# Kernel optimization log

Measured on AMD Instinct MI355X. Metric: run time of the kernel, lower is better.

Reference implementation:

```python
import jax, jax.numpy as jnp
import numpy as np

B, C, T = 32, 64, 8192
OUT, K = 129, 32
TWO_PI = 2.0 * np.pi
DROP_THRESH = 0.1  # squared-distance threshold for channel dropping


def setup_inputs() -> dict:
    key = jax.random.key(0)
    k1, k2, k3, k4, k5 = jax.random.split(key, 5)
    X = jax.random.normal(k1, (B, C, T), dtype=jnp.float32)
    positions = jax.random.uniform(k2, (B, C, 2), dtype=jnp.float32)
    drop_idx = jax.random.randint(k3, (B,), 0, C)
    scale = 1.0 / (K * K)
    z_real = jax.random.normal(k4, (OUT, K * K), dtype=jnp.float32) * scale
    z_imag = jax.random.normal(k5, (OUT, K * K), dtype=jnp.float32) * scale
    return {"X": X, "positions": positions, "drop_idx": drop_idx,
            "z_real": z_real, "z_imag": z_imag}


def reference(X, positions, drop_idx, z_real, z_imag):
    # frequency grid: feature index f = l_idx*K + k_idx (row-major over [l, k])
    kk = jnp.arange(1, K + 1, dtype=jnp.float32)
    coef_k = jnp.tile(kk, K)            # [K*K] varies fastest
    coef_l = jnp.repeat(kk, K)          # [K*K]

    x = positions[..., 0]               # [B, C]
    y = positions[..., 1]
    # phase: [B, C, K*K]
    phase = TWO_PI * (x[..., None] * coef_k + y[..., None] * coef_l)
    cos_mat = jnp.cos(phase)
    sin_mat = jnp.sin(phase)

    # a: [B, OUT, C]
    a = (jnp.einsum('of,bcf->boc', z_real, cos_mat)
         + jnp.einsum('of,bcf->boc', z_imag, sin_mat))

    # channel drop: remove all channels within sqdist < 0.1 of the dropped electrode
    pd = positions[jnp.arange(B), drop_idx]                 # [B, 2]
    dist = jnp.sum((positions - pd[:, None, :]) ** 2, axis=-1)  # [B, C]
    keep = dist >= DROP_THRESH                              # [B, C]

    a = jnp.where(keep[:, None, :], a, -1e9)
    attn = jax.nn.softmax(a, axis=2)                        # [B, OUT, C]
    # out: [B, OUT, T]
    return jnp.einsum('boc,bct->bot', attn, X)
```

## Files before the change

kernel.cpp:

```cpp
#include <hip/hip_runtime.h>
#include <math.h>

typedef __bf16 bf16x8 __attribute__((ext_vector_type(8)));
typedef unsigned short u16x8 __attribute__((ext_vector_type(8)));
typedef float f32x4 __attribute__((ext_vector_type(4)));

namespace {
constexpr int kB   = 32;
constexpr int kC   = 64;
constexpr int kT   = 8192;
constexpr int kOUT = 129;
constexpr int kKK  = 1024;
constexpr int kNKC = 8;
}

__device__ inline float sin2pi(float r) {
  float o; asm("v_sin_f32 %0, %1" : "=v"(o) : "v"(r)); return o;
}
__device__ inline float cos2pi(float r) {
  float o; asm("v_cos_f32 %0, %1" : "=v"(o) : "v"(r)); return o;
}
__device__ inline unsigned short f2bf_rne(float f) {
  unsigned int u = __builtin_bit_cast(unsigned int, f);
  return (unsigned short)((u + 0x7fffu + ((u >> 16) & 1u)) >> 16);
}
__device__ inline float bf2f(unsigned short h) {
  return __builtin_bit_cast(float, (unsigned int)h << 16);
}
__device__ inline void split8(const float* v, bf16x8& hi, bf16x8& lo) {
  u16x8 h, l;
#pragma unroll
  for (int j = 0; j < 8; ++j) {
    const unsigned short hh = f2bf_rne(v[j]);
    h[j] = hh;
    l[j] = f2bf_rne(v[j] - bf2f(hh));
  }
  hi = __builtin_bit_cast(bf16x8, h);
  lo = __builtin_bit_cast(bf16x8, l);
}

__global__ __launch_bounds__(256) void sa_phase_mfma(
    const float* __restrict__ positions,
    const float* __restrict__ z_real,
    const float* __restrict__ z_imag,
    float* __restrict__ part)
{
  const int bid = blockIdx.x;
  const int b   = bid & 31;
  const int kc  = (bid >> 5) & 7;
  const int mh  = bid >> 8;
  const int w    = threadIdx.x >> 6;
  const int lane = threadIdx.x & 63;
  const int cg   = lane >> 4;
  const int cl   = lane & 15;
  const int c    = w * 16 + cl;
  const int f0   = kc * 128;

  const float2 p = reinterpret_cast<const float2*>(positions)[b * kC + c];

  bf16x8 BcH[4], BcL[4], BsH[4], BsL[4];
#pragma unroll
  for (int ks = 0; ks < 4; ++ks) {
    float cs[8], sn[8];
#pragma unroll
    for (int j = 0; j < 8; ++j) {
      const int f = f0 + ks * 32 + 8 * cg + j;
      const float kf = (float)((f & 31) + 1);
      const float lf = (float)((f >> 5) + 1);
      const float wv = __fadd_rn(__fmul_rn(p.x, kf), __fmul_rn(p.y, lf));
      const float r  = wv - floorf(wv);
      cs[j] = cos2pi(r);
      sn[j] = sin2pi(r);
    }
    split8(cs, BcH[ks], BcL[ks]);
    split8(sn, BsH[ks], BsL[ks]);
  }

  const int nm  = mh ? 4 : 5;
  const int ob0 = mh * 80;

#pragma unroll
  for (int m = 0; m < 5; ++m) {
    if (m < nm) {
      const int ob = ob0 + m * 16;
      const int oa = ob + cl;
      bf16x8 ArH[4], ArL[4], AiH[4], AiL[4];
      if (oa < kOUT) {
        const float* zr = z_real + (size_t)oa * kKK + f0 + 8 * cg;
        const float* zi = z_imag + (size_t)oa * kKK + f0 + 8 * cg;
#pragma unroll
        for (int ks = 0; ks < 4; ++ks) {
          float vr[8], vi[8];
          *reinterpret_cast<float4*>(vr)     = *reinterpret_cast<const float4*>(zr + ks * 32);
          *reinterpret_cast<float4*>(vr + 4) = *reinterpret_cast<const float4*>(zr + ks * 32 + 4);
          *reinterpret_cast<float4*>(vi)     = *reinterpret_cast<const float4*>(zi + ks * 32);
          *reinterpret_cast<float4*>(vi + 4) = *reinterpret_cast<const float4*>(zi + ks * 32 + 4);
          split8(vr, ArH[ks], ArL[ks]);
          split8(vi, AiH[ks], AiL[ks]);
        }
      } else {
#pragma unroll
        for (int ks = 0; ks < 4; ++ks) {
          u16x8 z0 = {0,0,0,0,0,0,0,0};
          ArH[ks] = ArL[ks] = AiH[ks] = AiL[ks] = __builtin_bit_cast(bf16x8, z0);
        }
      }

      f32x4 acc = {0.f, 0.f, 0.f, 0.f};
#pragma unroll
      for (int ks = 0; ks < 4; ++ks) {
        acc = __builtin_amdgcn_mfma_f32_16x16x32_bf16(ArH[ks], BcH[ks], acc, 0, 0, 0);
        acc = __builtin_amdgcn_mfma_f32_16x16x32_bf16(ArH[ks], BcL[ks], acc, 0, 0, 0);
        acc = __builtin_amdgcn_mfma_f32_16x16x32_bf16(ArL[ks], BcH[ks], acc, 0, 0, 0);
        acc = __builtin_amdgcn_mfma_f32_16x16x32_bf16(AiH[ks], BsH[ks], acc, 0, 0, 0);
        acc = __builtin_amdgcn_mfma_f32_16x16x32_bf16(AiH[ks], BsL[ks], acc, 0, 0, 0);
        acc = __builtin_amdgcn_mfma_f32_16x16x32_bf16(AiL[ks], BsH[ks], acc, 0, 0, 0);
      }

#pragma unroll
      for (int r = 0; r < 4; ++r) {
        const int o = ob + cg * 4 + r;
        if (o < kOUT)
          part[(((size_t)kc * kB + b) * kOUT + o) * kC + c] = acc[r];
      }
    }
  }
}

__global__ __launch_bounds__(64) void sa_softmax(
    const float* __restrict__ part,
    const float* __restrict__ positions,
    const int*   __restrict__ drop_idx,
    unsigned short* __restrict__ a_hi,
    unsigned short* __restrict__ a_lo)
{
  const int bo = blockIdx.x;
  const int b  = bo / kOUT;
  const int o  = bo - b * kOUT;
  const int c  = threadIdx.x;

  float a = 0.f;
#pragma unroll
  for (int fc = 0; fc < kNKC; ++fc)
    a += part[(((size_t)fc * kB + b) * kOUT + o) * kC + c];

  const float2 p  = reinterpret_cast<const float2*>(positions)[b * kC + c];
  const int    di = drop_idx[b];
  const float2 pd = reinterpret_cast<const float2*>(positions)[b * kC + di];
  const float dx = p.x - pd.x;
  const float dy = p.y - pd.y;
  const float d2 = __fadd_rn(__fmul_rn(dx, dx), __fmul_rn(dy, dy));
  if (d2 < 0.1f) a = -1e9f;

  float m = a;
#pragma unroll
  for (int off = 32; off; off >>= 1) m = fmaxf(m, __shfl_xor(m, off));
  const float e = expf(a - m);
  float s = e;
#pragma unroll
  for (int off = 32; off; off >>= 1) s += __shfl_xor(s, off);

  const float att = e / s;
  const unsigned short h = f2bf_rne(att);
  const float res = att - bf2f(h);
  a_hi[((size_t)b * kOUT + o) * kC + c] = h;
  a_lo[((size_t)b * kOUT + o) * kC + c] = f2bf_rne(res);
}

__global__ __launch_bounds__(256) void sa_apply_mfma(
    const float* __restrict__ X,
    const unsigned short* __restrict__ a_hi,
    const unsigned short* __restrict__ a_lo,
    float* __restrict__ out)
{
  __shared__ unsigned short s_a[2 * 144 * kC];

  const int b   = blockIdx.x >> 6;
  const int tc  = blockIdx.x & 63;
  const int t0  = tc * 128;
  const int tid = threadIdx.x;

  {
    char* sb = reinterpret_cast<char*>(s_a);
    for (int i = tid; i < 2 * 144 * 8; i += 256) {
      const int tile = (i >= 144 * 8) ? 1 : 0;
      const int r    = (i >> 3) - tile * 144;
      const int ch   = i & 7;
      float4 v;
      if (r < kOUT) {
        const unsigned short* src =
            (tile ? a_lo : a_hi) + ((size_t)b * kOUT + r) * kC + ch * 8;
        v = *reinterpret_cast<const float4*>(src);
      } else {
        v = make_float4(0.f, 0.f, 0.f, 0.f);
      }
      const int byte = tile * (144 * 128) + r * 128 + ((ch * 16) ^ ((r & 7) << 4));
      *reinterpret_cast<float4*>(sb + byte) = v;
    }
  }

  const int wave = tid >> 6;
  const int lane = tid & 63;
  const int cl   = lane & 15;
  const int cg   = lane >> 4;
  const int tA   = t0 + wave * 32 + cl;
  const int tB   = tA + 16;

  const float* Xb = X + (size_t)b * kC * kT;
  float xvA[16], xvB[16];
#pragma unroll
  for (int s2 = 0; s2 < 2; ++s2)
#pragma unroll
    for (int j = 0; j < 8; ++j) {
      const size_t row = (size_t)(s2 * 32 + cg * 8 + j) * kT;
      xvA[s2 * 8 + j] = Xb[row + tA];
      xvB[s2 * 8 + j] = Xb[row + tB];
    }

  bf16x8 XhA0, XlA0, XhA1, XlA1, XhB0, XlB0, XhB1, XlB1;
  split8(xvA,     XhA0, XlA0);
  split8(xvA + 8, XhA1, XlA1);
  split8(xvB,     XhB0, XlB0);
  split8(xvB + 8, XhB1, XlB1);

  __syncthreads();

  const char* sb = reinterpret_cast<const char*>(s_a);
  float* outb = out + (size_t)b * kOUT * kT;

  for (int m = 0; m < 9; ++m) {
    const int row  = m * 16 + cl;
    const int base = row * 128;
    const int sw   = (row & 7) << 4;
    const int gb   = cg * 16;

    const bf16x8 Ah0 = *reinterpret_cast<const bf16x8*>(sb + base + ((gb     ) ^ sw));
    const bf16x8 Ah1 = *reinterpret_cast<const bf16x8*>(sb + base + ((gb + 64) ^ sw));
    const bf16x8 Al0 = *reinterpret_cast<const bf16x8*>(sb + 144 * 128 + base + ((gb     ) ^ sw));
    const bf16x8 Al1 = *reinterpret_cast<const bf16x8*>(sb + 144 * 128 + base + ((gb + 64) ^ sw));

    f32x4 accA = {0.f, 0.f, 0.f, 0.f};
    f32x4 accB = {0.f, 0.f, 0.f, 0.f};
    accA = __builtin_amdgcn_mfma_f32_16x16x32_bf16(Ah0, XhA0, accA, 0, 0, 0);
    accB = __builtin_amdgcn_mfma_f32_16x16x32_bf16(Ah0, XhB0, accB, 0, 0, 0);
    accA = __builtin_amdgcn_mfma_f32_16x16x32_bf16(Ah1, XhA1, accA, 0, 0, 0);
    accB = __builtin_amdgcn_mfma_f32_16x16x32_bf16(Ah1, XhB1, accB, 0, 0, 0);
    accA = __builtin_amdgcn_mfma_f32_16x16x32_bf16(Al0, XhA0, accA, 0, 0, 0);
    accB = __builtin_amdgcn_mfma_f32_16x16x32_bf16(Al0, XhB0, accB, 0, 0, 0);
    accA = __builtin_amdgcn_mfma_f32_16x16x32_bf16(Al1, XhA1, accA, 0, 0, 0);
    accB = __builtin_amdgcn_mfma_f32_16x16x32_bf16(Al1, XhB1, accB, 0, 0, 0);
    accA = __builtin_amdgcn_mfma_f32_16x16x32_bf16(Ah0, XlA0, accA, 0, 0, 0);
    accB = __builtin_amdgcn_mfma_f32_16x16x32_bf16(Ah0, XlB0, accB, 0, 0, 0);
    accA = __builtin_amdgcn_mfma_f32_16x16x32_bf16(Ah1, XlA1, accA, 0, 0, 0);
    accB = __builtin_amdgcn_mfma_f32_16x16x32_bf16(Ah1, XlB1, accB, 0, 0, 0);

#pragma unroll
    for (int r = 0; r < 4; ++r) {
      const int o = m * 16 + cg * 4 + r;
      if (o < kOUT) {
        outb[(size_t)o * kT + tA] = accA[r];
        outb[(size_t)o * kT + tB] = accB[r];
      }
    }
  }
}

extern "C" void kernel_launch(void* const* d_in, const int* in_sizes, int n_in,
                              void* d_out, int out_size, void* d_ws, size_t ws_size,
                              hipStream_t stream) {
  (void)in_sizes; (void)n_in; (void)out_size; (void)ws_size;
  const float* X         = (const float*)d_in[0];
  const float* positions = (const float*)d_in[1];
  const int*   drop_idx  = (const int*)d_in[2];
  const float* z_real    = (const float*)d_in[3];
  const float* z_imag    = (const float*)d_in[4];
  float* out = (float*)d_out;

  float* part = (float*)d_ws;
  unsigned short* ahi = (unsigned short*)(part + (size_t)kNKC * kB * kOUT * kC);
  unsigned short* alo = ahi + (size_t)kB * kOUT * kC;

  sa_phase_mfma<<<kB * kNKC * 2, 256, 0, stream>>>(positions, z_real, z_imag, part);
  sa_softmax<<<kB * kOUT, 64, 0, stream>>>(part, positions, drop_idx, ahi, alo);
  sa_apply_mfma<<<kB * 64, 256, 0, stream>>>(X, ahi, alo, out);
}
```

Baseline: 247.0 us.

## Precompute bf16 split operands in separate kernels and widen apply tiles

New measurement: 235.5 us. 1.05x faster.

```diff
diff --git a/kernel.cpp b/kernel.cpp
--- a/kernel.cpp
+++ b/kernel.cpp
@@ -12,6 +12,7 @@
 constexpr int kOUT = 129;
 constexpr int kKK  = 1024;
 constexpr int kNKC = 8;
+constexpr int kOP  = 144;
 }
 
 __device__ inline float sin2pi(float r) {
@@ -38,11 +39,61 @@
   hi = __builtin_bit_cast(bf16x8, h);
   lo = __builtin_bit_cast(bf16x8, l);
 }
-
-__global__ __launch_bounds__(256) void sa_phase_mfma(
+__device__ inline bf16x8 ldbf8(const unsigned short* p) {
+  return __builtin_bit_cast(bf16x8, *reinterpret_cast<const u16x8*>(p));
+}
+
+__global__ __launch_bounds__(256) void sa_split_z(
+    const float* __restrict__ z_real, const float* __restrict__ z_imag,
+    unsigned short* __restrict__ zrh, unsigned short* __restrict__ zrl,
+    unsigned short* __restrict__ zih, unsigned short* __restrict__ zil)
+{
+  const int i = blockIdx.x * 256 + threadIdx.x;
+  if (i >= 128 * kOP * 8) return;
+  const int fj = i & 7;
+  const int o  = (i >> 3) % kOP;
+  const int fb = i / (kOP * 8);
+  const int f  = fb * 8 + fj;
+  float vr = 0.f, vi = 0.f;
+  if (o < kOUT) {
+    vr = z_real[(size_t)o * kKK + f];
+    vi = z_imag[(size_t)o * kKK + f];
+  }
+  unsigned short h = f2bf_rne(vr);
+  zrh[i] = h; zrl[i] = f2bf_rne(vr - bf2f(h));
+  h = f2bf_rne(vi);
+  zih[i] = h; zil[i] = f2bf_rne(vi - bf2f(h));
+}
+
+__global__ __launch_bounds__(256) void sa_cis(
     const float* __restrict__ positions,
-    const float* __restrict__ z_real,
-    const float* __restrict__ z_imag,
+    unsigned short* __restrict__ csh, unsigned short* __restrict__ csl,
+    unsigned short* __restrict__ snh, unsigned short* __restrict__ snl)
+{
+  const int i = blockIdx.x * 256 + threadIdx.x;
+  const int fj = i & 7;
+  const int c  = (i >> 3) & 63;
+  const int fb = (i >> 9) & 127;
+  const int b  = i >> 16;
+  const int f  = fb * 8 + fj;
+  const float2 p = reinterpret_cast<const float2*>(positions)[b * kC + c];
+  const float kf = (float)((f & 31) + 1);
+  const float lf = (float)((f >> 5) + 1);
+  const float w = __fadd_rn(__fmul_rn(p.x, kf), __fmul_rn(p.y, lf));
+  const float r = w - floorf(w);
+  const float cs = cos2pi(r);
+  const float sn = sin2pi(r);
+  unsigned short h = f2bf_rne(cs);
+  csh[i] = h; csl[i] = f2bf_rne(cs - bf2f(h));
+  h = f2bf_rne(sn);
+  snh[i] = h; snl[i] = f2bf_rne(sn - bf2f(h));
+}
+
+__global__ __launch_bounds__(256) void sa_phase_gemm(
+    const unsigned short* __restrict__ zrh, const unsigned short* __restrict__ zrl,
+    const unsigned short* __restrict__ zih, const unsigned short* __restrict__ zil,
+    const unsigned short* __restrict__ csh, const unsigned short* __restrict__ csl,
+    const unsigned short* __restrict__ snh, const unsigned short* __restrict__ snl,
     float* __restrict__ part)
 {
   const int bid = blockIdx.x;
@@ -54,26 +105,15 @@
   const int cg   = lane >> 4;
   const int cl   = lane & 15;
   const int c    = w * 16 + cl;
-  const int f0   = kc * 128;
-
-  const float2 p = reinterpret_cast<const float2*>(positions)[b * kC + c];
 
   bf16x8 BcH[4], BcL[4], BsH[4], BsL[4];
 #pragma unroll
   for (int ks = 0; ks < 4; ++ks) {
-    float cs[8], sn[8];
-#pragma unroll
-    for (int j = 0; j < 8; ++j) {
-      const int f = f0 + ks * 32 + 8 * cg + j;
-      const float kf = (float)((f & 31) + 1);
-      const float lf = (float)((f >> 5) + 1);
-      const float wv = __fadd_rn(__fmul_rn(p.x, kf), __fmul_rn(p.y, lf));
-      const float r  = wv - floorf(wv);
-      cs[j] = cos2pi(r);
-      sn[j] = sin2pi(r);
-    }
-    split8(cs, BcH[ks], BcL[ks]);
-    split8(sn, BsH[ks], BsL[ks]);
+    const size_t off = ((size_t)(b * 128 + kc * 16 + ks * 4 + cg) * kC + c) * 8;
+    BcH[ks] = ldbf8(csh + off);
+    BcL[ks] = ldbf8(csl + off);
+    BsH[ks] = ldbf8(snh + off);
+    BsL[ks] = ldbf8(snl + off);
   }
 
   const int nm  = mh ? 4 : 5;
@@ -84,39 +124,21 @@
     if (m < nm) {
       const int ob = ob0 + m * 16;
       const int oa = ob + cl;
-      bf16x8 ArH[4], ArL[4], AiH[4], AiL[4];
-      if (oa < kOUT) {
-        const float* zr = z_real + (size_t)oa * kKK + f0 + 8 * cg;
-        const float* zi = z_imag + (size_t)oa * kKK + f0 + 8 * cg;
-#pragma unroll
-        for (int ks = 0; ks < 4; ++ks) {
-          float vr[8], vi[8];
-          *reinterpret_cast<float4*>(vr)     = *reinterpret_cast<const float4*>(zr + ks * 32);
-          *reinterpret_cast<float4*>(vr + 4) = *reinterpret_cast<const float4*>(zr + ks * 32 + 4);
-          *reinterpret_cast<float4*>(vi)     = *reinterpret_cast<const float4*>(zi + ks * 32);
-          *reinterpret_cast<float4*>(vi + 4) = *reinterpret_cast<const float4*>(zi + ks * 32 + 4);
-          split8(vr, ArH[ks], ArL[ks]);
-          split8(vi, AiH[ks], AiL[ks]);
-        }
-      } else {
-#pragma unroll
-        for (int ks = 0; ks < 4; ++ks) {
-          u16x8 z0 = {0,0,0,0,0,0,0,0};
-          ArH[ks] = ArL[ks] = AiH[ks] = AiL[ks] = __builtin_bit_cast(bf16x8, z0);
-        }
+      f32x4 acc = {0.f, 0.f, 0.f, 0.f};
+#pragma unroll
+      for (int ks = 0; ks < 4; ++ks) {
+        const size_t zo = ((size_t)(kc * 16 + ks * 4 + cg) * kOP + oa) * 8;
+        const bf16x8 ArH = ldbf8(zrh + zo);
+        const bf16x8 ArL = ldbf8(zrl + zo);
+        const bf16x8 AiH = ldbf8(zih + zo);
+        const bf16x8 AiL = ldbf8(zil + zo);
+        acc = __builtin_amdgcn_mfma_f32_16x16x32_bf16(ArH, BcH[ks], acc, 0, 0, 0);
+        acc = __builtin_amdgcn_mfma_f32_16x16x32_bf16(ArH, BcL[ks], acc, 0, 0, 0);
+        acc = __builtin_amdgcn_mfma_f32_16x16x32_bf16(ArL, BcH[ks], acc, 0, 0, 0);
+        acc = __builtin_amdgcn_mfma_f32_16x16x32_bf16(AiH, BsH[ks], acc, 0, 0, 0);
+        acc = __builtin_amdgcn_mfma_f32_16x16x32_bf16(AiH, BsL[ks], acc, 0, 0, 0);
+        acc = __builtin_amdgcn_mfma_f32_16x16x32_bf16(AiL, BsH[ks], acc, 0, 0, 0);
       }
-
-      f32x4 acc = {0.f, 0.f, 0.f, 0.f};
-#pragma unroll
-      for (int ks = 0; ks < 4; ++ks) {
-        acc = __builtin_amdgcn_mfma_f32_16x16x32_bf16(ArH[ks], BcH[ks], acc, 0, 0, 0);
-        acc = __builtin_amdgcn_mfma_f32_16x16x32_bf16(ArH[ks], BcL[ks], acc, 0, 0, 0);
-        acc = __builtin_amdgcn_mfma_f32_16x16x32_bf16(ArL[ks], BcH[ks], acc, 0, 0, 0);
-        acc = __builtin_amdgcn_mfma_f32_16x16x32_bf16(AiH[ks], BsH[ks], acc, 0, 0, 0);
-        acc = __builtin_amdgcn_mfma_f32_16x16x32_bf16(AiH[ks], BsL[ks], acc, 0, 0, 0);
-        acc = __builtin_amdgcn_mfma_f32_16x16x32_bf16(AiL[ks], BsH[ks], acc, 0, 0, 0);
-      }
-
 #pragma unroll
       for (int r = 0; r < 4; ++r) {
         const int o = ob + cg * 4 + r;
@@ -127,17 +149,18 @@
   }
 }
 
-__global__ __launch_bounds__(64) void sa_softmax(
+__global__ __launch_bounds__(256) void sa_softmax(
     const float* __restrict__ part,
     const float* __restrict__ positions,
     const int*   __restrict__ drop_idx,
     unsigned short* __restrict__ a_hi,
     unsigned short* __restrict__ a_lo)
 {
-  const int bo = blockIdx.x;
-  const int b  = bo / kOUT;
-  const int o  = bo - b * kOUT;
-  const int c  = threadIdx.x;
+  const int bo = blockIdx.x * 4 + (threadIdx.x >> 6);
+  if (bo >= kB * kOUT) return;
+  const int b = bo / kOUT;
+  const int o = bo - b * kOUT;
+  const int c = threadIdx.x & 63;
 
   float a = 0.f;
 #pragma unroll
@@ -162,9 +185,8 @@
 
   const float att = e / s;
   const unsigned short h = f2bf_rne(att);
-  const float res = att - bf2f(h);
-  a_hi[((size_t)b * kOUT + o) * kC + c] = h;
-  a_lo[((size_t)b * kOUT + o) * kC + c] = f2bf_rne(res);
+  a_hi[(size_t)bo * kC + c] = h;
+  a_lo[(size_t)bo * kC + c] = f2bf_rne(att - bf2f(h));
 }
 
 __global__ __launch_bounds__(256) void sa_apply_mfma(
@@ -175,9 +197,9 @@
 {
   __shared__ unsigned short s_a[2 * 144 * kC];
 
-  const int b   = blockIdx.x >> 6;
-  const int tc  = blockIdx.x & 63;
-  const int t0  = tc * 128;
+  const int b   = blockIdx.x >> 5;
+  const int tc  = blockIdx.x & 31;
+  const int t0  = tc * 256;
   const int tid = threadIdx.x;
 
   {
@@ -203,25 +225,22 @@
   const int lane = tid & 63;
   const int cl   = lane & 15;
   const int cg   = lane >> 4;
-  const int tA   = t0 + wave * 32 + cl;
-  const int tB   = tA + 16;
+  const int tb   = t0 + wave * 64;
 
   const float* Xb = X + (size_t)b * kC * kT;
-  float xvA[16], xvB[16];
-#pragma unroll
-  for (int s2 = 0; s2 < 2; ++s2)
-#pragma unroll
-    for (int j = 0; j < 8; ++j) {
-      const size_t row = (size_t)(s2 * 32 + cg * 8 + j) * kT;
-      xvA[s2 * 8 + j] = Xb[row + tA];
-      xvB[s2 * 8 + j] = Xb[row + tB];
-    }
-
-  bf16x8 XhA0, XlA0, XhA1, XlA1, XhB0, XlB0, XhB1, XlB1;
-  split8(xvA,     XhA0, XlA0);
-  split8(xvA + 8, XhA1, XlA1);
-  split8(xvB,     XhB0, XlB0);
-  split8(xvB + 8, XhB1, XlB1);
+  bf16x8 Xh[4][2], Xl[4][2];
+#pragma unroll
+  for (int n = 0; n < 4; ++n) {
+    const int t = tb + n * 16 + cl;
+    float xv[16];
+#pragma unroll
+    for (int s2 = 0; s2 < 2; ++s2)
+#pragma unroll
+      for (int j = 0; j < 8; ++j)
+        xv[s2 * 8 + j] = Xb[(size_t)(s2 * 32 + cg * 8 + j) * kT + t];
+    split8(xv,     Xh[n][0], Xl[n][0]);
+    split8(xv + 8, Xh[n][1], Xl[n][1]);
+  }
 
   __syncthreads();
 
@@ -239,29 +258,26 @@
     const bf16x8 Al0 = *reinterpret_cast<const bf16x8*>(sb + 144 * 128 + base + ((gb     ) ^ sw));
     const bf16x8 Al1 = *reinterpret_cast<const bf16x8*>(sb + 144 * 128 + base + ((gb + 64) ^ sw));
 
-    f32x4 accA = {0.f, 0.f, 0.f, 0.f};
-    f32x4 accB = {0.f, 0.f, 0.f, 0.f};
-    accA = __builtin_amdgcn_mfma_f32_16x16x32_bf16(Ah0, XhA0, accA, 0, 0, 0);
-    accB = __builtin_amdgcn_mfma_f32_16x16x32_bf16(Ah0, XhB0, accB, 0, 0, 0);
-    accA = __builtin_amdgcn_mfma_f32_16x16x32_bf16(Ah1, XhA1, accA, 0, 0, 0);
-    accB = __builtin_amdgcn_mfma_f32_16x16x32_bf16(Ah1, XhB1, accB, 0, 0, 0);
-    accA = __builtin_amdgcn_mfma_f32_16x16x32_bf16(Al0, XhA0, accA, 0, 0, 0);
-    accB = __builtin_amdgcn_mfma_f32_16x16x32_bf16(Al0, XhB0, accB, 0, 0, 0);
-    accA = __builtin_amdgcn_mfma_f32_16x16x32_bf16(Al1, XhA1, accA, 0, 0, 0);
-    accB = __builtin_amdgcn_mfma_f32_16x16x32_bf16(Al1, XhB1, accB, 0, 0, 0);
-    accA = __builtin_amdgcn_mfma_f32_16x16x32_bf16(Ah0, XlA0, accA, 0, 0, 0);
-    accB = __builtin_amdgcn_mfma_f32_16x16x32_bf16(Ah0, XlB0, accB, 0, 0, 0);
-    accA = __builtin_amdgcn_mfma_f32_16x16x32_bf16(Ah1, XlA1, accA, 0, 0, 0);
-    accB = __builtin_amdgcn_mfma_f32_16x16x32_bf16(Ah1, XlB1, accB, 0, 0, 0);
-
-#pragma unroll
-    for (int r = 0; r < 4; ++r) {
-      const int o = m * 16 + cg * 4 + r;
-      if (o < kOUT) {
-        outb[(size_t)o * kT + tA] = accA[r];
-        outb[(size_t)o * kT + tB] = accB[r];
+    f32x4 acc[4];
+#pragma unroll
+    for (int n = 0; n < 4; ++n) {
+      acc[n] = f32x4{0.f, 0.f, 0.f, 0.f};
+      acc[n] = __builtin_amdgcn_mfma_f32_16x16x32_bf16(Ah0, Xh[n][0], acc[n], 0, 0, 0);
+      acc[n] = __builtin_amdgcn_mfma_f32_16x16x32_bf16(Ah1, Xh[n][1], acc[n], 0, 0, 0);
+      acc[n] = __builtin_amdgcn_mfma_f32_16x16x32_bf16(Al0, Xh[n][0], acc[n], 0, 0, 0);
+      acc[n] = __builtin_amdgcn_mfma_f32_16x16x32_bf16(Al1, Xh[n][1], acc[n], 0, 0, 0);
+      acc[n] = __builtin_amdgcn_mfma_f32_16x16x32_bf16(Ah0, Xl[n][0], acc[n], 0, 0, 0);
+      acc[n] = __builtin_amdgcn_mfma_f32_16x16x32_bf16(Ah1, Xl[n][1], acc[n], 0, 0, 0);
+    }
+
+#pragma unroll
+    for (int n = 0; n < 4; ++n)
+#pragma unroll
+      for (int r = 0; r < 4; ++r) {
+        const int o = m * 16 + cg * 4 + r;
+        if (o < kOUT)
+          outb[(size_t)o * kT + tb + n * 16 + cl] = acc[n][r];
       }
-    }
   }
 }
 
@@ -276,11 +292,23 @@
   const float* z_imag    = (const float*)d_in[4];
   float* out = (float*)d_out;
 
-  float* part = (float*)d_ws;
-  unsigned short* ahi = (unsigned short*)(part + (size_t)kNKC * kB * kOUT * kC);
-  unsigned short* alo = ahi + (size_t)kB * kOUT * kC;
-
-  sa_phase_mfma<<<kB * kNKC * 2, 256, 0, stream>>>(positions, z_real, z_imag, part);
-  sa_softmax<<<kB * kOUT, 64, 0, stream>>>(part, positions, drop_idx, ahi, alo);
-  sa_apply_mfma<<<kB * 64, 256, 0, stream>>>(X, ahi, alo, out);
-}
+  char* wsb = (char*)d_ws;
+  float* part = (float*)wsb;
+  unsigned short* ahi = (unsigned short*)(wsb + 8454144);
+  unsigned short* alo = ahi + 264192;
+  unsigned short* zrh = alo + 264192;
+  unsigned short* zrl = zrh + 147456;
+  unsigned short* zih = zrl + 147456;
+  unsigned short* zil = zih + 147456;
+  unsigned short* csh = zil + 147456;
+  unsigned short* csl = csh + 2097152;
+  unsigned short* snh = csl + 2097152;
+  unsigned short* snl = snh + 2097152;
+
+  sa_split_z<<<576, 256, 0, stream>>>(z_real, z_imag, zrh, zrl, zih, zil);
+  sa_cis<<<8192, 256, 0, stream>>>(positions, csh, csl, snh, snl);
+  sa_phase_gemm<<<kB * kNKC * 2, 256, 0, stream>>>(zrh, zrl, zih, zil,
+                                                   csh, csl, snh, snl, part);
+  sa_softmax<<<(kB * kOUT + 3) / 4, 256, 0, stream>>>(part, positions, drop_idx, ahi, alo);
+  sa_apply_mfma<<<kB * 32, 256, 0, stream>>>(X, ahi, alo, out);
+}
```
